# Performance work log

Measured on AMD Instinct MI355X. Metric: run time of the kernel, lower is better.

Reference implementation:

```python
import jax, jax.numpy as jnp
import numpy as np

V, E, H, L, B, T = 32000, 512, 512, 4, 32, 64

def setup_inputs() -> dict:
    key = jax.random.key(0)
    ks = jax.random.split(key, 12)
    s = 0.04  # ~1/sqrt(H), matches torch LSTMCell uniform scale magnitude
    emb = jax.random.normal(ks[0], (V, E), jnp.float32) * s
    emb = emb.at[0].set(0.0)  # padding_idx=0
    return {
        'context': jax.random.normal(ks[1], (B, T, H), jnp.float32),
        'dec_input': jax.random.randint(ks[2], (B, T), 0, V),
        'h0': jax.random.normal(ks[3], (L, B, H), jnp.float32) * s,
        'c0': jax.random.normal(ks[4], (L, B, H), jnp.float32) * s,
        'emb': emb,
        'W_ih': jax.random.normal(ks[5], (L, 4 * H, E), jnp.float32) * s,
        'W_hh': jax.random.normal(ks[6], (L, 4 * H, H), jnp.float32) * s,
        'b_ih': jax.random.normal(ks[7], (L, 4 * H), jnp.float32) * s,
        'b_hh': jax.random.normal(ks[8], (L, 4 * H), jnp.float32) * s,
        'W_cls': jax.random.normal(ks[9], (V, H), jnp.float32) * s,
        'b_cls': jax.random.normal(ks[10], (V,), jnp.float32) * s,
    }

def _stack_lstm_scan(x, h0, c0, W_ih, W_hh, b_ih, b_hh):
    # x: [B,T,E] -> scan over time with L stacked LSTMCells + residual
    n_layers = W_ih.shape[0]

    def step(carry, x_t):
        h, c = carry  # each [L,B,H]
        inp = x_t
        new_h, new_c = [], []
        for i in range(n_layers):
            gates = inp @ W_ih[i].T + b_ih[i] + h[i] @ W_hh[i].T + b_hh[i]
            ig, fg, gg, og = jnp.split(gates, 4, axis=-1)  # torch order: i,f,g,o
            ci = jax.nn.sigmoid(fg) * c[i] + jax.nn.sigmoid(ig) * jnp.tanh(gg)
            hi = jax.nn.sigmoid(og) * jnp.tanh(ci)
            # residual when dims match (E == H here)
            inp = hi + inp if inp.shape[-1] == hi.shape[-1] else hi
            new_h.append(hi)
            new_c.append(ci)
        return (jnp.stack(new_h), jnp.stack(new_c)), inp

    (hT, cT), outs = jax.lax.scan(step, (h0, c0), jnp.swapaxes(x, 0, 1))
    return jnp.swapaxes(outs, 0, 1), hT, cT  # [B,T,H]

def reference(context, dec_input, h0, c0, emb, W_ih, W_hh, b_ih, b_hh, W_cls, b_cls):
    x = emb[dec_input]  # [B,T,E]; dropouts are identity (p=0 / eval)
    outs, hT, cT = _stack_lstm_scan(x, h0, c0, W_ih, W_hh, b_ih, b_hh)
    logits = outs @ W_cls.T + b_cls  # [B,T,V]
    # original applies log_softmax over dim=1 (the sequence dim) - faithful
    out = jax.nn.log_softmax(logits, axis=1)
    return (out, hT, cT)
```

## Files before the change

### kernel.cpp

```cpp
#include <hip/hip_runtime.h>
#include <math.h>

#define VOCAB 32000
#define HDIM  512
#define NLAYERS 4
#define BATCH 32
#define TSTEPS 64
typedef unsigned long long ULL;

typedef __attribute__((ext_vector_type(8))) short bf16x8;
typedef __attribute__((ext_vector_type(4))) float f32x4;
typedef __attribute__((ext_vector_type(4))) unsigned int u32x4;

static __device__ __forceinline__ unsigned short f2b(float f) {
    union { float f; unsigned u; } v; v.f = f;
    return (unsigned short)((v.u + 0x7FFFu + ((v.u >> 16) & 1u)) >> 16);
}
static __device__ __forceinline__ float sigf(float x) { return 1.0f / (1.0f + __expf(-x)); }

static __device__ __forceinline__ int apack_off(int m, int k) {
    int k0 = k >> 5, mi = m >> 4;
    int lane = (m & 15) | (((k >> 3) & 3) << 4);
    return ((k0 * 2 + mi) * 64 + lane) * 8 + (k & 7);
}

__global__ void k_prep_w(const float* __restrict__ W_ih, const float* __restrict__ W_hh,
                         unsigned short* __restrict__ wp) {
    const int total = NLAYERS * 64 * 2 * 32 * 64 * 8;
    for (int idx = blockIdx.x * blockDim.x + threadIdx.x; idx < total;
         idx += gridDim.x * blockDim.x) {
        int sub = idx & 7, lane = (idx >> 3) & 63, k0 = (idx >> 9) & 31;
        int ni = (idx >> 14) & 1, bi = (idx >> 15) & 63, l = idx >> 21;
        int r = ni * 16 + (lane & 15);
        int k = k0 * 32 + ((lane >> 4) << 3) + sub;
        int j = (r & 3) * 512 + bi * 8 + (r >> 2);
        float v = (k < 512) ? W_ih[((size_t)l * 2048 + j) * 512 + k]
                            : W_hh[((size_t)l * 2048 + j) * 512 + (k - 512)];
        wp[idx] = f2b(v);
    }
}

__global__ void k_prep_bias(const float* __restrict__ b_ih, const float* __restrict__ b_hh,
                            float* __restrict__ bs) {
    int idx = blockIdx.x * blockDim.x + threadIdx.x;
    if (idx < NLAYERS * 64 * 32) {
        int r = idx & 31, bi = (idx >> 5) & 63, l = idx >> 11;
        int j = (r & 3) * 512 + bi * 8 + (r >> 2);
        bs[idx] = b_ih[l * 2048 + j] + b_hh[l * 2048 + j];
    }
}

__global__ void k_prep_wcls(const float* __restrict__ W_cls, unsigned short* __restrict__ wp) {
    int idx8 = blockIdx.x * blockDim.x + threadIdx.x;
    int lane = idx8 & 63, k0 = (idx8 >> 6) & 15, ni = (idx8 >> 10) & 1;
    int w = (idx8 >> 11) & 3, vt = idx8 >> 13;
    int v = vt * 128 + w * 32 + ni * 16 + (lane & 15);
    int kb = k0 * 32 + ((lane >> 4) << 3);
    const float* src = W_cls + (size_t)v * 512 + kb;
    float4 f0 = *(const float4*)(src);
    float4 f1 = *(const float4*)(src + 4);
    bf16x8 u;
    u[0] = (short)f2b(f0.x); u[1] = (short)f2b(f0.y);
    u[2] = (short)f2b(f0.z); u[3] = (short)f2b(f0.w);
    u[4] = (short)f2b(f1.x); u[5] = (short)f2b(f1.y);
    u[6] = (short)f2b(f1.z); u[7] = (short)f2b(f1.w);
    *(bf16x8*)(wp + (size_t)idx8 * 8) = u;
}

__global__ void k_embed(const float* __restrict__ emb, const int* __restrict__ dec,
                        float* __restrict__ seqF, unsigned short* __restrict__ seqBp) {
    int t = blockIdx.x;
    for (int i = threadIdx.x; i < BATCH * HDIM; i += blockDim.x) {
        int b = i >> 9, e = i & 511;
        int tok = dec[b * TSTEPS + t];
        float v = emb[(size_t)tok * HDIM + e];
        seqF[((size_t)t * BATCH + b) * HDIM + e] = v;
        seqBp[(size_t)t * 16384 + apack_off(b, e)] = f2b(v);
    }
}

__global__ void k_inith(const float* __restrict__ h0, unsigned short* __restrict__ apack) {
    int idx = blockIdx.x * blockDim.x + threadIdx.x;
    int l = idx >> 14, b = (idx >> 9) & 31, d = idx & 511;
    apack[(size_t)(l * 2) * 32768 + apack_off(b, 512 + d)] =
        f2b(h0[((size_t)l * BATCH + b) * HDIM + d]);
}

__global__ __launch_bounds__(256, 1) void k_lstm(
    unsigned short* apack,
    const unsigned short* __restrict__ wpack,
    const float* __restrict__ bsum,
    const unsigned short* __restrict__ seqBp,
    const float* __restrict__ seqF,
    float* outF,
    unsigned short* __restrict__ seqOut,
    const float* __restrict__ c0,
    float* __restrict__ outHT, float* __restrict__ outCT,
    unsigned* flags) {
    const int l = blockIdx.x >> 6, bi = blockIdx.x & 63;
    const int wave = threadIdx.x >> 6, lane = threadIdx.x & 63;
    const int mi = wave >> 1, ni = wave & 1;
    const int cb = threadIdx.x >> 3, dsl = threadIdx.x & 7;
    const int d = bi * 8 + dsl;

    __shared__ __align__(16) short sW[32768];
    __shared__ __align__(16) short sA[32768];
    __shared__ __align__(16) float sG[1024];
    __shared__ __align__(16) short sHexH[512];
    __shared__ __align__(16) short sHexO[512];

    {
        const unsigned short* wp = wpack + (size_t)blockIdx.x * 32768;
        #pragma unroll
        for (int i = 0; i < 16; ++i) {
            int off = (i * 256 + threadIdx.x) * 8;
            *(bf16x8*)(sW + off) = *(const bf16x8*)(wp + off);
        }
    }
    float4 bias = *(const float4*)(bsum + blockIdx.x * 32 + dsl * 4);
    float c = c0[((size_t)l * BATCH + cb) * HDIM + d];

    unsigned short* A0 = apack + (size_t)(l * 2 + 0) * 32768;
    unsigned short* A1 = apack + (size_t)(l * 2 + 1) * 32768;

    for (int t = 0; t < TSTEPS; ++t) {
        if (l == 0) {
            const unsigned short* sp = seqBp + (size_t)t * 16384;
            #pragma unroll
            for (int i = 0; i < 8; ++i) {
                int off = (i * 256 + threadIdx.x) * 8;
                *(bf16x8*)(sA + off) = *(const bf16x8*)(sp + off);
            }
        }

        if (wave == 0 && t > 0) {
            const unsigned* fp = flags + (l * 64 + lane) * 16;
            while (__hip_atomic_load(fp, __ATOMIC_RELAXED, __HIP_MEMORY_SCOPE_AGENT)
                   < (unsigned)t)
                __builtin_amdgcn_s_sleep(1);
        }
        if (wave == 1 && l > 0) {
            const unsigned* fp = flags + ((l - 1) * 64 + lane) * 16;
            while (__hip_atomic_load(fp, __ATOMIC_RELAXED, __HIP_MEMORY_SCOPE_AGENT)
                   < (unsigned)(t + 1))
                __builtin_amdgcn_s_sleep(1);
        }
        if (wave == 2 && l < 3 && t > 0) {
            const unsigned* fp = flags + ((l + 1) * 64 + lane) * 16;
            while (__hip_atomic_load(fp, __ATOMIC_RELAXED, __HIP_MEMORY_SCOPE_AGENT)
                   < (unsigned)(t - 1))
                __builtin_amdgcn_s_sleep(1);
        }
        __syncthreads();

        float inpf;
        if (l == 0) inpf = seqF[((size_t)t * BATCH + cb) * HDIM + d];
        else inpf = __hip_atomic_load(&outF[(size_t)((l * 2 + (t & 1)) * BATCH + cb) * HDIM + d],
                                      __ATOMIC_RELAXED, __HIP_MEMORY_SCOPE_AGENT);

        const unsigned short* Ab = (t & 1) ? A1 : A0;
        const ULL* Abu = (const ULL*)Ab;
        ULL* sAu = (ULL*)sA;
        if (l == 0) {
            ULL tmp[16];
            #pragma unroll
            for (int i = 0; i < 16; ++i)
                tmp[i] = __hip_atomic_load(&Abu[(16 + i) * 256 + threadIdx.x],
                                           __ATOMIC_RELAXED, __HIP_MEMORY_SCOPE_AGENT);
            #pragma unroll
            for (int i = 0; i < 16; ++i)
                sAu[(16 + i) * 256 + threadIdx.x] = tmp[i];
        } else {
            ULL tmp[32];
            #pragma unroll
            for (int i = 0; i < 32; ++i)
                tmp[i] = __hip_atomic_load(&Abu[i * 256 + threadIdx.x],
                                           __ATOMIC_RELAXED, __HIP_MEMORY_SCOPE_AGENT);
            #pragma unroll
            for (int i = 0; i < 32; ++i)
                sAu[i * 256 + threadIdx.x] = tmp[i];
        }
        __syncthreads();

        f32x4 acc = {0.f, 0.f, 0.f, 0.f};
        const short* abase = sA + mi * 512 + lane * 8;
        const short* wbase = sW + ni * 16384 + lane * 8;
        #pragma unroll
        for (int k0 = 0; k0 < 32; ++k0)
            acc = __builtin_amdgcn_mfma_f32_16x16x32_bf16(
                *(const bf16x8*)(abase + k0 * 1024),
                *(const bf16x8*)(wbase + k0 * 512), acc, 0, 0, 0);

        int gb = mi * 16 + (lane >> 4) * 4;
        int gr = ni * 16 + (lane & 15);
        #pragma unroll
        for (int r = 0; r < 4; ++r) sG[(gb + r) * 32 + gr] = acc[r];
        __syncthreads();

        float4 g4 = *(const float4*)(sG + cb * 32 + dsl * 4);
        float gi = g4.x + bias.x, gf = g4.y + bias.y;
        float gg = g4.z + bias.z, go = g4.w + bias.w;
        float ci = sigf(gf) * c + sigf(gi) * tanhf(gg);
        float hi = sigf(go) * tanhf(ci);
        c = ci;
        float o = hi + inpf;

        sHexH[threadIdx.x] = f2b(hi);
        sHexO[threadIdx.x] = f2b(o);
        if (l < 3)
            __hip_atomic_store(&outF[(size_t)(((l + 1) * 2 + (t & 1)) * BATCH + cb) * HDIM + d],
                               o, __ATOMIC_RELAXED, __HIP_MEMORY_SCOPE_AGENT);
        if (t == TSTEPS - 1) {
            outHT[((size_t)l * BATCH + cb) * HDIM + d] = hi;
            outCT[((size_t)l * BATCH + cb) * HDIM + d] = ci;
        }
        __syncthreads();

        unsigned short* An = ((t + 1) & 1) ? A1 : A0;
        int i = threadIdx.x & 63, cbe = i >> 1, jh = i & 1;
        int lanecode = ((cbe & 15) | ((bi & 3) << 4)) * 2 + jh;
        if (threadIdx.x < 64) {
            int hoff = ((16 + (bi >> 2)) * 2 + (cbe >> 4)) * 128 + lanecode;
            __hip_atomic_store(&((ULL*)An)[hoff], ((const ULL*)sHexH)[i],
                               __ATOMIC_RELAXED, __HIP_MEMORY_SCOPE_AGENT);
        } else if (threadIdx.x < 128) {
            if (l < 3) {
                unsigned short* Anx = apack + (size_t)((l + 1) * 2 + (t & 1)) * 32768;
                int ooff = ((bi >> 2) * 2 + (cbe >> 4)) * 128 + lanecode;
                __hip_atomic_store(&((ULL*)Anx)[ooff], ((const ULL*)sHexO)[i],
                                   __ATOMIC_RELAXED, __HIP_MEMORY_SCOPE_AGENT);
            } else {
                int ulidx = ((((cbe * 16 + (bi >> 2)) * 4 + (t >> 4)) * 64 +
                             ((t & 15) | ((bi & 3) << 4))) * 2) + jh;
                ((ULL*)seqOut)[ulidx] = ((const ULL*)sHexO)[i];
            }
        }

        asm volatile("s_waitcnt vmcnt(0)" ::: "memory");
        __syncthreads();
        if (threadIdx.x == 0)
            __hip_atomic_store(&flags[(l * 64 + bi) * 16], (unsigned)(t + 1),
                               __ATOMIC_RELAXED, __HIP_MEMORY_SCOPE_AGENT);
    }
}

__global__ __launch_bounds__(256) void k_cls(
    const unsigned short* __restrict__ Ap,
    const unsigned short* __restrict__ Wp,
    float* __restrict__ out) {
    int b = blockIdx.x & 31;
    int vt = blockIdx.x >> 5;
    int wave = threadIdx.x >> 6;
    int lane = threadIdx.x & 63;

    __shared__ float sL[64 * 132];

    const unsigned short* abase = Ap + (size_t)b * 32768 + lane * 8;
    const unsigned short* wbase = Wp + (size_t)(vt * 4 + wave) * 16384 + lane * 8;

    f32x4 acc[4][2];
    #pragma unroll
    for (int i = 0; i < 4; ++i)
        #pragma unroll
        for (int j = 0; j < 2; ++j) acc[i][j] = (f32x4)(0.0f);

    #pragma unroll 4
    for (int k0 = 0; k0 < 16; ++k0) {
        bf16x8 a[4], bb[2];
        #pragma unroll
        for (int mi = 0; mi < 4; ++mi)
            a[mi] = *(const bf16x8*)(abase + (k0 * 4 + mi) * 512);
        #pragma unroll
        for (int ni = 0; ni < 2; ++ni)
            bb[ni] = *(const bf16x8*)(wbase + ni * 8192 + k0 * 512);
        #pragma unroll
        for (int mi = 0; mi < 4; ++mi)
            #pragma unroll
            for (int ni = 0; ni < 2; ++ni)
                acc[mi][ni] = __builtin_amdgcn_mfma_f32_16x16x32_bf16(a[mi], bb[ni], acc[mi][ni], 0, 0, 0);
    }

    #pragma unroll
    for (int ni = 0; ni < 2; ++ni) {
        float m = -1e30f;
        #pragma unroll
        for (int mi = 0; mi < 4; ++mi)
            #pragma unroll
            for (int r = 0; r < 4; ++r) m = fmaxf(m, acc[mi][ni][r]);
        m = fmaxf(m, __shfl_xor(m, 16));
        m = fmaxf(m, __shfl_xor(m, 32));
        float s = 0.f;
        #pragma unroll
        for (int mi = 0; mi < 4; ++mi)
            #pragma unroll
            for (int r = 0; r < 4; ++r) s += expf(acc[mi][ni][r] - m);
        s += __shfl_xor(s, 16);
        s += __shfl_xor(s, 32);
        float logZ = m + logf(s);
        int col = wave * 32 + ni * 16 + (lane & 15);
        #pragma unroll
        for (int mi = 0; mi < 4; ++mi) {
            #pragma unroll
            for (int r = 0; r < 4; ++r) {
                int row = mi * 16 + (lane >> 4) * 4 + r;
                sL[row * 132 + col] = acc[mi][ni][r] - logZ;
            }
        }
    }
    __syncthreads();

    float* obase = out + (size_t)b * TSTEPS * VOCAB + vt * 128;
    #pragma unroll
    for (int it = 0; it < 8; ++it) {
        int idx = it * 256 + threadIdx.x;
        int row = idx >> 5, c4 = (idx & 31) * 4;
        float4 val = *(const float4*)(sL + row * 132 + c4);
        *(float4*)(obase + (size_t)row * VOCAB + c4) = val;
    }
}

extern "C" void kernel_launch(void* const* d_in, const int* in_sizes, int n_in,
                              void* d_out, int out_size, void* d_ws, size_t ws_size,
                              hipStream_t stream) {
    const int*   dec   = (const int*)d_in[1];
    const float* h0    = (const float*)d_in[2];
    const float* c0    = (const float*)d_in[3];
    const float* emb   = (const float*)d_in[4];
    const float* W_ih  = (const float*)d_in[5];
    const float* W_hh  = (const float*)d_in[6];
    const float* b_ih  = (const float*)d_in[7];
    const float* b_hh  = (const float*)d_in[8];
    const float* W_cls = (const float*)d_in[9];

    const int LBH = NLAYERS * BATCH * HDIM;
    const size_t BTV = (size_t)BATCH * TSTEPS * VOCAB;

    char* ws = (char*)d_ws;
    size_t off = 0;
    auto alloc = [&](size_t bytes) -> void* {
        void* p = ws + off;
        off = (off + bytes + 255) & ~(size_t)255;
        return p;
    };
    unsigned short* wpack  = (unsigned short*)alloc((size_t)NLAYERS * 64 * 2 * 32 * 64 * 8 * 2);
    float*          bsum   = (float*)alloc((size_t)NLAYERS * 64 * 32 * 4);
    unsigned short* wpackC = (unsigned short*)alloc((size_t)VOCAB * HDIM * 2);
    float*          seqF   = (float*)alloc((size_t)TSTEPS * BATCH * HDIM * 4);
    unsigned short* seqBp  = (unsigned short*)alloc((size_t)TSTEPS * 16384 * 2);
    unsigned short* apack  = (unsigned short*)alloc((size_t)NLAYERS * 2 * 32768 * 2);
    float*          outF   = (float*)alloc((size_t)NLAYERS * 2 * BATCH * HDIM * 4);
    unsigned short* apackC = (unsigned short*)alloc((size_t)TSTEPS * BATCH * HDIM * 2);
    unsigned*       flags  = (unsigned*)alloc(16384);

    k_prep_w<<<4096, 256, 0, stream>>>(W_ih, W_hh, wpack);
    k_prep_bias<<<32, 256, 0, stream>>>(b_ih, b_hh, bsum);
    k_prep_wcls<<<8000, 256, 0, stream>>>(W_cls, wpackC);
    k_embed<<<TSTEPS, 256, 0, stream>>>(emb, dec, seqF, seqBp);
    k_inith<<<256, 256, 0, stream>>>(h0, apack);
    hipMemsetAsync(flags, 0, 16384, stream);

    k_lstm<<<256, 256, 0, stream>>>(apack, wpack, bsum, seqBp, seqF, outF, apackC,
                                    c0,
                                    (float*)d_out + BTV,
                                    (float*)d_out + BTV + LBH,
                                    flags);

    k_cls<<<250 * 32, 256, 0, stream>>>(apackC, wpackC, (float*)d_out);
}
```

Baseline: 489.7 us.

## Merge prep kernels into one launch; classifier handles two batches per block

```diff
diff --git a/kernel.cpp b/kernel.cpp
--- a/kernel.cpp
+++ b/kernel.cpp
@@ -24,66 +24,67 @@
     return ((k0 * 2 + mi) * 64 + lane) * 8 + (k & 7);
 }
 
-__global__ void k_prep_w(const float* __restrict__ W_ih, const float* __restrict__ W_hh,
-                         unsigned short* __restrict__ wp) {
-    const int total = NLAYERS * 64 * 2 * 32 * 64 * 8;
-    for (int idx = blockIdx.x * blockDim.x + threadIdx.x; idx < total;
-         idx += gridDim.x * blockDim.x) {
-        int sub = idx & 7, lane = (idx >> 3) & 63, k0 = (idx >> 9) & 31;
-        int ni = (idx >> 14) & 1, bi = (idx >> 15) & 63, l = idx >> 21;
-        int r = ni * 16 + (lane & 15);
-        int k = k0 * 32 + ((lane >> 4) << 3) + sub;
-        int j = (r & 3) * 512 + bi * 8 + (r >> 2);
-        float v = (k < 512) ? W_ih[((size_t)l * 2048 + j) * 512 + k]
-                            : W_hh[((size_t)l * 2048 + j) * 512 + (k - 512)];
-        wp[idx] = f2b(v);
-    }
-}
-
-__global__ void k_prep_bias(const float* __restrict__ b_ih, const float* __restrict__ b_hh,
-                            float* __restrict__ bs) {
-    int idx = blockIdx.x * blockDim.x + threadIdx.x;
-    if (idx < NLAYERS * 64 * 32) {
-        int r = idx & 31, bi = (idx >> 5) & 63, l = idx >> 11;
-        int j = (r & 3) * 512 + bi * 8 + (r >> 2);
-        bs[idx] = b_ih[l * 2048 + j] + b_hh[l * 2048 + j];
-    }
-}
-
-__global__ void k_prep_wcls(const float* __restrict__ W_cls, unsigned short* __restrict__ wp) {
-    int idx8 = blockIdx.x * blockDim.x + threadIdx.x;
-    int lane = idx8 & 63, k0 = (idx8 >> 6) & 15, ni = (idx8 >> 10) & 1;
-    int w = (idx8 >> 11) & 3, vt = idx8 >> 13;
-    int v = vt * 128 + w * 32 + ni * 16 + (lane & 15);
-    int kb = k0 * 32 + ((lane >> 4) << 3);
-    const float* src = W_cls + (size_t)v * 512 + kb;
-    float4 f0 = *(const float4*)(src);
-    float4 f1 = *(const float4*)(src + 4);
-    bf16x8 u;
-    u[0] = (short)f2b(f0.x); u[1] = (short)f2b(f0.y);
-    u[2] = (short)f2b(f0.z); u[3] = (short)f2b(f0.w);
-    u[4] = (short)f2b(f1.x); u[5] = (short)f2b(f1.y);
-    u[6] = (short)f2b(f1.z); u[7] = (short)f2b(f1.w);
-    *(bf16x8*)(wp + (size_t)idx8 * 8) = u;
-}
-
-__global__ void k_embed(const float* __restrict__ emb, const int* __restrict__ dec,
-                        float* __restrict__ seqF, unsigned short* __restrict__ seqBp) {
-    int t = blockIdx.x;
-    for (int i = threadIdx.x; i < BATCH * HDIM; i += blockDim.x) {
-        int b = i >> 9, e = i & 511;
-        int tok = dec[b * TSTEPS + t];
-        float v = emb[(size_t)tok * HDIM + e];
-        seqF[((size_t)t * BATCH + b) * HDIM + e] = v;
-        seqBp[(size_t)t * 16384 + apack_off(b, e)] = f2b(v);
-    }
-}
-
-__global__ void k_inith(const float* __restrict__ h0, unsigned short* __restrict__ apack) {
-    int idx = blockIdx.x * blockDim.x + threadIdx.x;
-    int l = idx >> 14, b = (idx >> 9) & 31, d = idx & 511;
-    apack[(size_t)(l * 2) * 32768 + apack_off(b, 512 + d)] =
-        f2b(h0[((size_t)l * BATCH + b) * HDIM + d]);
+__global__ void k_prep_all(
+    const float* __restrict__ W_ih, const float* __restrict__ W_hh,
+    const float* __restrict__ b_ih, const float* __restrict__ b_hh,
+    const float* __restrict__ W_cls, const float* __restrict__ emb,
+    const int* __restrict__ dec, const float* __restrict__ h0,
+    unsigned short* __restrict__ wp, float* __restrict__ bs,
+    unsigned short* __restrict__ wpC, float* __restrict__ seqF,
+    unsigned short* __restrict__ seqBp, unsigned short* __restrict__ apack,
+    unsigned* __restrict__ flags) {
+    int blk = blockIdx.x;
+    if (blk < 4096) {
+        const int total = NLAYERS * 64 * 2 * 32 * 64 * 8;
+        for (int idx = blk * 256 + threadIdx.x; idx < total; idx += 4096 * 256) {
+            int sub = idx & 7, lane = (idx >> 3) & 63, k0 = (idx >> 9) & 31;
+            int ni = (idx >> 14) & 1, bi = (idx >> 15) & 63, l = idx >> 21;
+            int r = ni * 16 + (lane & 15);
+            int k = k0 * 32 + ((lane >> 4) << 3) + sub;
+            int j = (r & 3) * 512 + bi * 8 + (r >> 2);
+            float v = (k < 512) ? W_ih[((size_t)l * 2048 + j) * 512 + k]
+                                : W_hh[((size_t)l * 2048 + j) * 512 + (k - 512)];
+            wp[idx] = f2b(v);
+        }
+    } else if (blk < 12096) {
+        int idx8 = (blk - 4096) * 256 + threadIdx.x;
+        int lane = idx8 & 63, k0 = (idx8 >> 6) & 15, ni = (idx8 >> 10) & 1;
+        int w = (idx8 >> 11) & 3, vt = idx8 >> 13;
+        int v = vt * 128 + w * 32 + ni * 16 + (lane & 15);
+        int kb = k0 * 32 + ((lane >> 4) << 3);
+        const float* src = W_cls + (size_t)v * 512 + kb;
+        float4 f0 = *(const float4*)(src);
+        float4 f1 = *(const float4*)(src + 4);
+        bf16x8 u;
+        u[0] = (short)f2b(f0.x); u[1] = (short)f2b(f0.y);
+        u[2] = (short)f2b(f0.z); u[3] = (short)f2b(f0.w);
+        u[4] = (short)f2b(f1.x); u[5] = (short)f2b(f1.y);
+        u[6] = (short)f2b(f1.z); u[7] = (short)f2b(f1.w);
+        *(bf16x8*)(wpC + (size_t)idx8 * 8) = u;
+    } else if (blk < 12160) {
+        int t = blk - 12096;
+        for (int i = threadIdx.x; i < BATCH * HDIM; i += blockDim.x) {
+            int b = i >> 9, e = i & 511;
+            int tok = dec[b * TSTEPS + t];
+            float v = emb[(size_t)tok * HDIM + e];
+            seqF[((size_t)t * BATCH + b) * HDIM + e] = v;
+            seqBp[(size_t)t * 16384 + apack_off(b, e)] = f2b(v);
+        }
+    } else if (blk < 12416) {
+        int idx = (blk - 12160) * 256 + threadIdx.x;
+        int l = idx >> 14, b = (idx >> 9) & 31, d = idx & 511;
+        apack[(size_t)(l * 2) * 32768 + apack_off(b, 512 + d)] =
+            f2b(h0[((size_t)l * BATCH + b) * HDIM + d]);
+    } else if (blk < 12448) {
+        int idx = (blk - 12416) * 256 + threadIdx.x;
+        if (idx < NLAYERS * 64 * 32) {
+            int r = idx & 31, bi = (idx >> 5) & 63, l = idx >> 11;
+            int j = (r & 3) * 512 + bi * 8 + (r >> 2);
+            bs[idx] = b_ih[l * 2048 + j] + b_hh[l * 2048 + j];
+        }
+    } else {
+        for (int i = threadIdx.x; i < 4096; i += 256) flags[i] = 0;
+    }
 }
 
 __global__ __launch_bounds__(256, 1) void k_lstm(
@@ -248,74 +249,84 @@
     const unsigned short* __restrict__ Ap,
     const unsigned short* __restrict__ Wp,
     float* __restrict__ out) {
-    int b = blockIdx.x & 31;
-    int vt = blockIdx.x >> 5;
+    int bp = blockIdx.x & 15;
+    int vt = blockIdx.x >> 4;
     int wave = threadIdx.x >> 6;
     int lane = threadIdx.x & 63;
 
     __shared__ float sL[64 * 132];
 
-    const unsigned short* abase = Ap + (size_t)b * 32768 + lane * 8;
+    const unsigned short* abase = Ap + (size_t)(bp * 2) * 32768 + lane * 8;
     const unsigned short* wbase = Wp + (size_t)(vt * 4 + wave) * 16384 + lane * 8;
 
-    f32x4 acc[4][2];
+    f32x4 acc[2][4][2];
     #pragma unroll
-    for (int i = 0; i < 4; ++i)
-        #pragma unroll
-        for (int j = 0; j < 2; ++j) acc[i][j] = (f32x4)(0.0f);
-
-    #pragma unroll 4
+    for (int s = 0; s < 2; ++s)
+        #pragma unroll
+        for (int i = 0; i < 4; ++i)
+            #pragma unroll
+            for (int j = 0; j < 2; ++j) acc[s][i][j] = (f32x4)(0.0f);
+
     for (int k0 = 0; k0 < 16; ++k0) {
-        bf16x8 a[4], bb[2];
-        #pragma unroll
-        for (int mi = 0; mi < 4; ++mi)
-            a[mi] = *(const bf16x8*)(abase + (k0 * 4 + mi) * 512);
+        bf16x8 bb[2];
         #pragma unroll
         for (int ni = 0; ni < 2; ++ni)
             bb[ni] = *(const bf16x8*)(wbase + ni * 8192 + k0 * 512);
         #pragma unroll
-        for (int mi = 0; mi < 4; ++mi)
-            #pragma unroll
-            for (int ni = 0; ni < 2; ++ni)
-                acc[mi][ni] = __builtin_amdgcn_mfma_f32_16x16x32_bf16(a[mi], bb[ni], acc[mi][ni], 0, 0, 0);
+        for (int s = 0; s < 2; ++s) {
+            bf16x8 a[4];
+            #pragma unroll
+            for (int mi = 0; mi < 4; ++mi)
+                a[mi] = *(const bf16x8*)(abase + s * 32768 + (k0 * 4 + mi) * 512);
+            #pragma unroll
+            for (int mi = 0; mi < 4; ++mi)
+                #pragma unroll
+                for (int ni = 0; ni < 2; ++ni)
+                    acc[s][mi][ni] = __builtin_amdgcn_mfma_f32_16x16x32_bf16(
+                        a[mi], bb[ni], acc[s][mi][ni], 0, 0, 0);
+        }
     }
 
     #pragma unroll
-    for (int ni = 0; ni < 2; ++ni) {
-        float m = -1e30f;
-        #pragma unroll
-        for (int mi = 0; mi < 4; ++mi)
-            #pragma unroll
-            for (int r = 0; r < 4; ++r) m = fmaxf(m, acc[mi][ni][r]);
-        m = fmaxf(m, __shfl_xor(m, 16));
-        m = fmaxf(m, __shfl_xor(m, 32));
-        float s = 0.f;
-        #pragma unroll
-        for (int mi = 0; mi < 4; ++mi)
-            #pragma unroll
-            for (int r = 0; r < 4; ++r) s += expf(acc[mi][ni][r] - m);
-        s += __shfl_xor(s, 16);
-        s += __shfl_xor(s, 32);
-        float logZ = m + logf(s);
-        int col = wave * 32 + ni * 16 + (lane & 15);
-        #pragma unroll
-        for (int mi = 0; mi < 4; ++mi) {
-            #pragma unroll
-            for (int r = 0; r < 4; ++r) {
-                int row = mi * 16 + (lane >> 4) * 4 + r;
-                sL[row * 132 + col] = acc[mi][ni][r] - logZ;
+    for (int s = 0; s < 2; ++s) {
+        if (s) __syncthreads();
+        #pragma unroll
+        for (int ni = 0; ni < 2; ++ni) {
+            float m = -1e30f;
+            #pragma unroll
+            for (int mi = 0; mi < 4; ++mi)
+                #pragma unroll
+                for (int r = 0; r < 4; ++r) m = fmaxf(m, acc[s][mi][ni][r]);
+            m = fmaxf(m, __shfl_xor(m, 16));
+            m = fmaxf(m, __shfl_xor(m, 32));
+            float sum = 0.f;
+            #pragma unroll
+            for (int mi = 0; mi < 4; ++mi)
+                #pragma unroll
+                for (int r = 0; r < 4; ++r) sum += expf(acc[s][mi][ni][r] - m);
+            sum += __shfl_xor(sum, 16);
+            sum += __shfl_xor(sum, 32);
+            float logZ = m + logf(sum);
+            int col = wave * 32 + ni * 16 + (lane & 15);
+            #pragma unroll
+            for (int mi = 0; mi < 4; ++mi) {
+                #pragma unroll
+                for (int r = 0; r < 4; ++r) {
+                    int row = mi * 16 + (lane >> 4) * 4 + r;
+                    sL[row * 132 + col] = acc[s][mi][ni][r] - logZ;
+                }
             }
         }
-    }
-    __syncthreads();
-
-    float* obase = out + (size_t)b * TSTEPS * VOCAB + vt * 128;
-    #pragma unroll
-    for (int it = 0; it < 8; ++it) {
-        int idx = it * 256 + threadIdx.x;
-        int row = idx >> 5, c4 = (idx & 31) * 4;
-        float4 val = *(const float4*)(sL + row * 132 + c4);
-        *(float4*)(obase + (size_t)row * VOCAB + c4) = val;
+        __syncthreads();
+
+        float* obase = out + (size_t)(bp * 2 + s) * TSTEPS * VOCAB + vt * 128;
+        #pragma unroll
+        for (int it = 0; it < 8; ++it) {
+            int idx = it * 256 + threadIdx.x;
+            int row = idx >> 5, c4 = (idx & 31) * 4;
+            f32x4 val = *(const f32x4*)(sL + row * 132 + c4);
+            __builtin_nontemporal_store(val, (f32x4*)(obase + (size_t)row * VOCAB + c4));
+        }
     }
 }
 
@@ -352,12 +363,8 @@
     unsigned short* apackC = (unsigned short*)alloc((size_t)TSTEPS * BATCH * HDIM * 2);
     unsigned*       flags  = (unsigned*)alloc(16384);
 
-    k_prep_w<<<4096, 256, 0, stream>>>(W_ih, W_hh, wpack);
-    k_prep_bias<<<32, 256, 0, stream>>>(b_ih, b_hh, bsum);
-    k_prep_wcls<<<8000, 256, 0, stream>>>(W_cls, wpackC);
-    k_embed<<<TSTEPS, 256, 0, stream>>>(emb, dec, seqF, seqBp);
-    k_inith<<<256, 256, 0, stream>>>(h0, apack);
-    hipMemsetAsync(flags, 0, 16384, stream);
+    k_prep_all<<<12449, 256, 0, stream>>>(W_ih, W_hh, b_ih, b_hh, W_cls, emb, dec, h0,
+                                          wpack, bsum, wpackC, seqF, seqBp, apack, flags);
 
     k_lstm<<<256, 256, 0, stream>>>(apack, wpack, bsum, seqBp, seqF, outF, apackC,
                                     c0,
@@ -365,5 +372,5 @@
                                     (float*)d_out + BTV + LBH,
                                     flags);
 
-    k_cls<<<250 * 32, 256, 0, stream>>>(apackC, wpackC, (float*)d_out);
-}
+    k_cls<<<250 * 16, 256, 0, stream>>>(apackC, wpackC, (float*)d_out);
+}
```

Result: faster. 458.4 us (-6.4%).
